# Performance work log

Hardware: AMD Instinct MI355X
Metric: run time of the kernel (lower is better)

The kernel has to match this reference:

```python
import jax, jax.numpy as jnp
import numpy as np

OUT_FEATURES = 4096
IN_FEATURES = 4096
GROUP_SIZE = 128
NUMEL = OUT_FEATURES * IN_FEATURES  # 16777216


def setup_inputs() -> dict:
    key = jax.random.key(0)
    k1, k2, k3, k4, k5 = jax.random.split(key, 5)
    x = jax.random.normal(k1, (4, 2048, IN_FEATURES), dtype=jnp.float32)
    # two int4 values packed per byte -> NUMEL // 2 bytes
    packed = jax.random.randint(k2, (NUMEL // 2,), 0, 256, dtype=jnp.int32)
    # per-group scale/offset (NUMEL // GROUP_SIZE groups)
    scales = jax.random.uniform(k3, (NUMEL // GROUP_SIZE,), dtype=jnp.float32) * 0.1 + 1e-3
    offsets = jax.random.normal(k4, (NUMEL // GROUP_SIZE,), dtype=jnp.float32) * 0.01
    bias = jax.random.normal(k5, (OUT_FEATURES,), dtype=jnp.float32)
    return {"x": x, "packed": packed, "scales": scales, "offsets": offsets, "bias": bias}


def int4_dequantize(packed, scales, offsets):
    # low nibble, then high nibble, interleaved: [l0, h0, l1, h1, ...]
    low = packed & 15
    high = (packed >> 4) & 15
    q = jnp.stack([low, high], axis=1).reshape(-1).astype(jnp.float32)  # [NUMEL]
    groups = q.reshape(-1, GROUP_SIZE)  # [n_groups, group_size]
    w = groups * scales[:, None] + offsets[:, None]
    return w.reshape(OUT_FEATURES, IN_FEATURES)


def reference(x, packed, scales, offsets, bias):
    w = int4_dequantize(packed, scales, offsets)  # [out, in]
    # F.linear: y = x @ w.T + bias
    return jnp.einsum('bsi,oi->bso', x, w) + bias
```

## Files before the change

kernel.cpp:

```cpp
#include <hip/hip_runtime.h>
#include <stdint.h>

typedef __attribute__((ext_vector_type(4))) float  f32x4;
typedef __attribute__((ext_vector_type(4))) int    i32x4;
typedef __attribute__((ext_vector_type(8))) __bf16 bf16x8;

constexpr int M_DIM = 8192, N_DIM = 4096, K_DIM = 4096;

#define VMCNT(n) asm volatile("s_waitcnt vmcnt(" #n ")" ::: "memory")
#define LGKMCNT0 asm volatile("s_waitcnt lgkmcnt(0)" ::: "memory")

__global__ __launch_bounds__(256) void cvt_x(const float* __restrict__ X,
                                             __bf16* __restrict__ Xb) {
  size_t i = ((size_t)blockIdx.x * 256 + threadIdx.x) * 8;
  const f32x4* src = (const f32x4*)(X + i);
  f32x4 a = src[0], b = src[1];
  bf16x8 v;
  v[0] = (__bf16)a[0]; v[1] = (__bf16)a[1]; v[2] = (__bf16)a[2]; v[3] = (__bf16)a[3];
  v[4] = (__bf16)b[0]; v[5] = (__bf16)b[1]; v[6] = (__bf16)b[2]; v[7] = (__bf16)b[3];
  *(bf16x8*)(Xb + i) = v;
}

__global__ __launch_bounds__(256) void deq_w(const int* __restrict__ P,
                                             const float* __restrict__ S,
                                             const float* __restrict__ O,
                                             __bf16* __restrict__ Wb) {
  size_t i = (size_t)blockIdx.x * 256 + threadIdx.x;
  const i32x4* src = (const i32x4*)(P + i * 16);
  int g = (int)(i >> 2);
  float s = S[g], o = O[g];
  __bf16* dst = Wb + i * 32;
#pragma unroll
  for (int j = 0; j < 4; ++j) {
    i32x4 p = src[j];
    bf16x8 v;
#pragma unroll
    for (int b = 0; b < 4; ++b) {
      int pv = p[b];
      v[2 * b]     = (__bf16)fmaf((float)(pv & 15), s, o);
      v[2 * b + 1] = (__bf16)fmaf((float)((pv >> 4) & 15), s, o);
    }
    *(bf16x8*)(dst + j * 8) = v;
  }
}

__device__ __forceinline__ void stage64(const char* g, size_t rs, char* l, int tid) {
  const int r = tid >> 3;
  const int c = ((tid & 7) * 16) ^ ((r & 7) << 4);
  __builtin_amdgcn_global_load_lds(
      (const __attribute__((address_space(1))) uint32_t*)(g + (size_t)r * rs + c),
      (__attribute__((address_space(3))) uint32_t*)(l + (tid >> 6) * 1024),
      16, 0, 0);
}

__global__ __launch_bounds__(512, 2) void gemm8(const __bf16* __restrict__ A,
                                                const __bf16* __restrict__ B,
                                                const float* __restrict__ Bias,
                                                float* __restrict__ Y) {
  extern __shared__ char lds[];

  constexpr int NT = K_DIM / 64;
  const int tid  = threadIdx.x;
  const int lane = tid & 63;
  const int wid  = tid >> 6;
  const int wm   = wid >> 2;
  const int wn   = wid & 3;
  const int ln15 = lane & 15;
  const int lq   = lane >> 4;
  const int bn0  = blockIdx.x * 256;
  const int bm0  = blockIdx.y * 256;
  const size_t rs = (size_t)K_DIM * 2;

  const char* Ag = (const char*)A + (size_t)bm0 * rs;
  const char* Bg = (const char*)B + (size_t)bn0 * rs;

  f32x4 acc[8][4];
#pragma unroll
  for (int m = 0; m < 8; ++m)
#pragma unroll
    for (int n = 0; n < 4; ++n)
      acc[m][n] = (f32x4){0.f, 0.f, 0.f, 0.f};

  {
    char* Ab = lds;
    char* Bb = lds + 65536;
    stage64(Bg + (size_t)0 * rs,   rs, Bb + 0,     tid);
    stage64(Bg + (size_t)64 * rs,  rs, Bb + 8192,  tid);
    stage64(Bg + (size_t)128 * rs, rs, Bb + 16384, tid);
    stage64(Bg + (size_t)192 * rs, rs, Bb + 24576, tid);
    stage64(Ag + (size_t)0 * rs,   rs, Ab + 0,     tid);
    stage64(Ag + (size_t)128 * rs, rs, Ab + 16384, tid);
    stage64(Ag + (size_t)64 * rs,  rs, Ab + 8192,  tid);
    stage64(Ag + (size_t)192 * rs, rs, Ab + 24576, tid);
  }
  VMCNT(2);
  __builtin_amdgcn_s_barrier();

  for (int t = 0; t < NT; ++t) {
    const char* Ab = lds + (t & 1) * 32768;
    const char* Bb = lds + 65536 + (t & 1) * 32768;
    char* An = lds + ((t + 1) & 1) * 32768;
    char* Bn = lds + 65536 + ((t + 1) & 1) * 32768;
    const bool st = (t + 1 < NT);
    const char* ga = Ag + (size_t)(t + 1) * 128;
    const char* gb = Bg + (size_t)(t + 1) * 128;

#pragma unroll
    for (int q = 0; q < 4; ++q) {
      const int mh = q >> 1, nh = q & 1;
      __builtin_amdgcn_sched_barrier(0);

      bf16x8 af[4][2], bfr[2][2];
#pragma unroll
      for (int m4 = 0; m4 < 4; ++m4) {
        const int r  = wm * 128 + (mh * 4 + m4) * 16 + ln15;
        const int sw = (r & 7) << 4;
#pragma unroll
        for (int ks = 0; ks < 2; ++ks)
          af[m4][ks] = *(const bf16x8*)(Ab + r * 128 + ((ks * 64 + lq * 16) ^ sw));
      }
#pragma unroll
      for (int n2 = 0; n2 < 2; ++n2) {
        const int r  = wn * 64 + (nh * 2 + n2) * 16 + ln15;
        const int sw = (r & 7) << 4;
#pragma unroll
        for (int ks = 0; ks < 2; ++ks)
          bfr[n2][ks] = *(const bf16x8*)(Bb + r * 128 + ((ks * 64 + lq * 16) ^ sw));
      }

      if (st) {
        if (q == 0) { stage64(gb, rs, Bn, tid);
                      stage64(gb + (size_t)64 * rs, rs, Bn + 8192, tid); }
        if (q == 1) { stage64(gb + (size_t)128 * rs, rs, Bn + 16384, tid);
                      stage64(gb + (size_t)192 * rs, rs, Bn + 24576, tid); }
        if (q == 2) { stage64(ga, rs, An, tid);
                      stage64(ga + (size_t)128 * rs, rs, An + 16384, tid); }
        if (q == 3) { stage64(ga + (size_t)64 * rs, rs, An + 8192, tid);
                      stage64(ga + (size_t)192 * rs, rs, An + 24576, tid); }
      }

      __builtin_amdgcn_s_barrier();
      LGKMCNT0;
      __builtin_amdgcn_sched_barrier(0);

      __builtin_amdgcn_s_setprio(1);
#pragma unroll
      for (int ks = 0; ks < 2; ++ks)
#pragma unroll
        for (int m4 = 0; m4 < 4; ++m4)
#pragma unroll
          for (int n2 = 0; n2 < 2; ++n2)
            acc[mh * 4 + m4][nh * 2 + n2] = __builtin_amdgcn_mfma_f32_16x16x32_bf16(
                af[m4][ks], bfr[n2][ks], acc[mh * 4 + m4][nh * 2 + n2], 0, 0, 0);
      __builtin_amdgcn_s_setprio(0);
      __builtin_amdgcn_sched_barrier(0);

      if (q == 1) {
        if (t == NT - 1) { VMCNT(0); } else { VMCNT(4); }
      }
      if (q == 3) { VMCNT(2); }
      __builtin_amdgcn_s_barrier();
    }
  }

#pragma unroll
  for (int n = 0; n < 4; ++n) {
    const int col = bn0 + wn * 64 + n * 16 + ln15;
    const float bias = Bias[col];
#pragma unroll
    for (int m = 0; m < 8; ++m) {
      const int row0 = bm0 + wm * 128 + m * 16 + lq * 4;
#pragma unroll
      for (int r = 0; r < 4; ++r)
        Y[(size_t)(row0 + r) * N_DIM + col] = acc[m][n][r] + bias;
    }
  }
}

__global__ __launch_bounds__(256) void qlin_fused_gemm(
    const float* __restrict__ X, const int* __restrict__ P,
    const float* __restrict__ S, const float* __restrict__ Ofs,
    const float* __restrict__ Bias, float* __restrict__ Y)
{
  constexpr int BM = 128, BN = 128, BK = 64;
  constexpr int NT = K_DIM / BK;
  __shared__ __bf16 As[BM * BK];
  __shared__ __bf16 Bs[BN * BK];

  const int tid  = threadIdx.x;
  const int lane = tid & 63;
  const int wv   = tid >> 6;
  const int wr   = (wv >> 1) * 64;
  const int wc   = (wv & 1) * 64;
  const int bn0 = blockIdx.x * BN;
  const int bm0 = blockIdx.y * BM;
  const int srow  = tid >> 1;
  const int shalf = tid & 1;

  const float* xrow = X + (size_t)(bm0 + srow) * K_DIM + shalf * 32;
  const int*   prow = P + (size_t)(bn0 + srow) * (K_DIM / 2) + shalf * 16;
  const int    gbase = (bn0 + srow) * (K_DIM / 128);

  const int rowb = srow * (BK * 2);
  const int sxor = (srow & 7) << 4;
  const int cbb  = shalf * 64;

  f32x4 areg[8];
  i32x4 breg[4];
  float sc, of;

  f32x4 acc[4][4];
#pragma unroll
  for (int i = 0; i < 4; ++i)
#pragma unroll
    for (int j = 0; j < 4; ++j)
      acc[i][j] = (f32x4){0.f, 0.f, 0.f, 0.f};

#pragma unroll
  for (int i = 0; i < 8; ++i) areg[i] = *(const f32x4*)(xrow + 4 * i);
#pragma unroll
  for (int i = 0; i < 4; ++i) breg[i] = *(const i32x4*)(prow + 4 * i);
  sc = S[gbase];
  of = Ofs[gbase];

  for (int kt = 0; kt < NT; ++kt) {
    __syncthreads();
    {
      char* ab = (char*)As + rowb;
      char* bb = (char*)Bs + rowb;
#pragma unroll
      for (int i = 0; i < 4; ++i) {
        bf16x8 v;
        f32x4 u0 = areg[2 * i], u1 = areg[2 * i + 1];
        v[0] = (__bf16)u0[0]; v[1] = (__bf16)u0[1];
        v[2] = (__bf16)u0[2]; v[3] = (__bf16)u0[3];
        v[4] = (__bf16)u1[0]; v[5] = (__bf16)u1[1];
        v[6] = (__bf16)u1[2]; v[7] = (__bf16)u1[3];
        *(bf16x8*)(ab + ((cbb + 16 * i) ^ sxor)) = v;
      }
#pragma unroll
      for (int i = 0; i < 4; ++i) {
        bf16x8 v;
        i32x4 p = breg[i];
#pragma unroll
        for (int j = 0; j < 4; ++j) {
          int pv = p[j];
          v[2 * j]     = (__bf16)fmaf((float)(pv & 15), sc, of);
          v[2 * j + 1] = (__bf16)fmaf((float)((pv >> 4) & 15), sc, of);
        }
        *(bf16x8*)(bb + ((cbb + 16 * i) ^ sxor)) = v;
      }
    }
    if (kt + 1 < NT) {
      const float* xp = xrow + (kt + 1) * BK;
#pragma unroll
      for (int i = 0; i < 8; ++i) areg[i] = *(const f32x4*)(xp + 4 * i);
      const int* pp = prow + (kt + 1) * (BK / 2);
#pragma unroll
      for (int i = 0; i < 4; ++i) breg[i] = *(const i32x4*)(pp + 4 * i);
      int g = gbase + (kt + 1) / 2;
      sc = S[g]; of = Ofs[g];
    }
    __syncthreads();
#pragma unroll
    for (int ks = 0; ks < 2; ++ks) {
      const int cb = ks * 64 + (lane >> 4) * 16;
      bf16x8 afr[4], bfr[4];
#pragma unroll
      for (int m = 0; m < 4; ++m) {
        int r = wr + m * 16 + (lane & 15);
        afr[m] = *(const bf16x8*)((const char*)As + r * (BK * 2) + (cb ^ ((r & 7) << 4)));
      }
#pragma unroll
      for (int n = 0; n < 4; ++n) {
        int r = wc + n * 16 + (lane & 15);
        bfr[n] = *(const bf16x8*)((const char*)Bs + r * (BK * 2) + (cb ^ ((r & 7) << 4)));
      }
#pragma unroll
      for (int m = 0; m < 4; ++m)
#pragma unroll
        for (int n = 0; n < 4; ++n)
          acc[m][n] = __builtin_amdgcn_mfma_f32_16x16x32_bf16(afr[m], bfr[n], acc[m][n], 0, 0, 0);
    }
  }
#pragma unroll
  for (int n = 0; n < 4; ++n) {
    const int col = bn0 + wc + n * 16 + (lane & 15);
    const float bias = Bias[col];
#pragma unroll
    for (int m = 0; m < 4; ++m) {
      const int row0 = bm0 + wr + m * 16 + (lane >> 4) * 4;
#pragma unroll
      for (int r = 0; r < 4; ++r)
        Y[(size_t)(row0 + r) * N_DIM + col] = acc[m][n][r] + bias;
    }
  }
}

extern "C" void kernel_launch(void* const* d_in, const int* in_sizes, int n_in,
                              void* d_out, int out_size, void* d_ws, size_t ws_size,
                              hipStream_t stream) {
  const float* X    = (const float*)d_in[0];
  const int*   P    = (const int*)d_in[1];
  const float* S    = (const float*)d_in[2];
  const float* Ofs  = (const float*)d_in[3];
  const float* Bias = (const float*)d_in[4];
  float* Y = (float*)d_out;

  const size_t xb_bytes = (size_t)M_DIM * K_DIM * 2;
  const size_t wb_bytes = (size_t)N_DIM * K_DIM * 2;

  if (ws_size >= xb_bytes + wb_bytes) {
    __bf16* Xb = (__bf16*)d_ws;
    __bf16* Wb = (__bf16*)((char*)d_ws + xb_bytes);

    cvt_x<<<dim3((M_DIM * K_DIM) / (256 * 8)), dim3(256), 0, stream>>>(X, Xb);
    deq_w<<<dim3((N_DIM * K_DIM) / (256 * 32)), dim3(256), 0, stream>>>(P, S, Ofs, Wb);

    hipFuncSetAttribute((const void*)gemm8,
                        hipFuncAttributeMaxDynamicSharedMemorySize, 131072);
    dim3 grid(N_DIM / 256, M_DIM / 256);
    gemm8<<<grid, dim3(512), 131072, stream>>>(Xb, Wb, Bias, Y);
  } else {
    dim3 grid(N_DIM / 128, M_DIM / 128);
    qlin_fused_gemm<<<grid, dim3(256), 0, stream>>>(X, P, S, Ofs, Bias, Y);
  }
}
```

Measured before the change: 307.6 us.

## Remap blocks per XCD and split GEMM inner loop by k-step to reuse B fragments

Block IDs are permuted so that the blocks assigned round-robin to the same XCD cover a contiguous range of output tiles, aiming for better L2 reuse of the A and B panels. The inner quadrant loop is reorganised to iterate over the two k-halves and two M-halves. B fragments are loaded once per k-half and reused across both M-halves, which roughly halves LDS fragment reads per tile. The vmcnt waits are retimed to match the new order in which A rows are read. The remap assumes the fixed 16x32 grid, and the tighter wait schedule could add stalls or ordering risk.

```diff
diff --git a/kernel.cpp b/kernel.cpp
--- a/kernel.cpp
+++ b/kernel.cpp
@@ -67,10 +67,13 @@
   const int wn   = wid & 3;
   const int ln15 = lane & 15;
   const int lq   = lane >> 4;
-  const int bn0  = blockIdx.x * 256;
-  const int bm0  = blockIdx.y * 256;
+
+  const int id  = blockIdx.y * gridDim.x + blockIdx.x;
+  const int swz = (id & 7) * 64 + (id >> 3);
+  const int bn0 = (swz & 15) * 256;
+  const int bm0 = (swz >> 4) * 256;
+
   const size_t rs = (size_t)K_DIM * 2;
-
   const char* Ag = (const char*)A + (size_t)bm0 * rs;
   const char* Bg = (const char*)B + (size_t)bn0 * rs;
 
@@ -105,27 +108,27 @@
     const char* ga = Ag + (size_t)(t + 1) * 128;
     const char* gb = Bg + (size_t)(t + 1) * 128;
 
+    bf16x8 bfr[4];
+
 #pragma unroll
     for (int q = 0; q < 4; ++q) {
-      const int mh = q >> 1, nh = q & 1;
+      const int mh = q & 1, ks = q >> 1;
       __builtin_amdgcn_sched_barrier(0);
 
-      bf16x8 af[4][2], bfr[2][2];
+      if (mh == 0) {
+#pragma unroll
+        for (int n = 0; n < 4; ++n) {
+          const int r  = wn * 64 + n * 16 + ln15;
+          const int sw = (r & 7) << 4;
+          bfr[n] = *(const bf16x8*)(Bb + r * 128 + ((ks * 64 + lq * 16) ^ sw));
+        }
+      }
+      bf16x8 af[4];
 #pragma unroll
       for (int m4 = 0; m4 < 4; ++m4) {
         const int r  = wm * 128 + (mh * 4 + m4) * 16 + ln15;
         const int sw = (r & 7) << 4;
-#pragma unroll
-        for (int ks = 0; ks < 2; ++ks)
-          af[m4][ks] = *(const bf16x8*)(Ab + r * 128 + ((ks * 64 + lq * 16) ^ sw));
-      }
-#pragma unroll
-      for (int n2 = 0; n2 < 2; ++n2) {
-        const int r  = wn * 64 + (nh * 2 + n2) * 16 + ln15;
-        const int sw = (r & 7) << 4;
-#pragma unroll
-        for (int ks = 0; ks < 2; ++ks)
-          bfr[n2][ks] = *(const bf16x8*)(Bb + r * 128 + ((ks * 64 + lq * 16) ^ sw));
+        af[m4] = *(const bf16x8*)(Ab + r * 128 + ((ks * 64 + lq * 16) ^ sw));
       }
 
       if (st) {
@@ -145,20 +148,18 @@
 
       __builtin_amdgcn_s_setprio(1);
 #pragma unroll
-      for (int ks = 0; ks < 2; ++ks)
-#pragma unroll
-        for (int m4 = 0; m4 < 4; ++m4)
-#pragma unroll
-          for (int n2 = 0; n2 < 2; ++n2)
-            acc[mh * 4 + m4][nh * 2 + n2] = __builtin_amdgcn_mfma_f32_16x16x32_bf16(
-                af[m4][ks], bfr[n2][ks], acc[mh * 4 + m4][nh * 2 + n2], 0, 0, 0);
+      for (int m4 = 0; m4 < 4; ++m4)
+#pragma unroll
+        for (int n = 0; n < 4; ++n)
+          acc[mh * 4 + m4][n] = __builtin_amdgcn_mfma_f32_16x16x32_bf16(
+              af[m4], bfr[n], acc[mh * 4 + m4][n], 0, 0, 0);
       __builtin_amdgcn_s_setprio(0);
       __builtin_amdgcn_sched_barrier(0);
 
-      if (q == 1) {
-        if (t == NT - 1) { VMCNT(0); } else { VMCNT(4); }
-      }
-      if (q == 3) { VMCNT(2); }
+      if (q == 0) {
+        if (t == NT - 1) { VMCNT(0); } else { VMCNT(2); }
+      }
+      if (q == 3 && st) { VMCNT(2); }
       __builtin_amdgcn_s_barrier();
     }
   }
```

After: 275.4 us. -10.5%, faster.
